# Kernel optimization log

Measured on AMD Instinct MI355X. Metric: run time of the kernel, lower is better.

The kernel has to match this reference:

```python
import jax, jax.numpy as jnp
import numpy as np

MAX_POINTS = 32
EPS = 1e-5


def setup_inputs() -> dict:
    key = jax.random.key(0)
    k1, k2, k3, k4, k5, k6 = jax.random.split(key, 6)
    M, P, C_IN, C_OUT = 40000, MAX_POINTS, 4, 64
    voxel_features = jax.random.normal(k1, (M, P, C_IN), dtype=jnp.float32)
    voxel_num_points = jax.random.randint(k2, (M,), 0, MAX_POINTS, dtype=jnp.int32)
    # Linear(C_in, C_out) params (PyTorch default init scale ~ U(-1/sqrt(fan_in), ...))
    lim = 1.0 / np.sqrt(C_IN)
    W = jax.random.uniform(k3, (C_OUT, C_IN), minval=-lim, maxval=lim, dtype=jnp.float32)
    b = jax.random.uniform(k4, (C_OUT,), minval=-lim, maxval=lim, dtype=jnp.float32)
    # BatchNorm1d affine params
    gamma = jnp.ones((C_OUT,), dtype=jnp.float32)
    beta = jnp.zeros((C_OUT,), dtype=jnp.float32)
    return {"voxel_features": voxel_features, "voxel_num_points": voxel_num_points,
            "W": W, "b": b, "gamma": gamma, "beta": beta}


def _vfe(x, n, W, b, gamma, beta):
    # x: (M, P, C_in), n: (M,) valid point counts
    mask = (jnp.arange(MAX_POINTS)[None, :] < n[:, None])            # (M, P)
    maskf = mask.astype(x.dtype)[..., None]                          # (M, P, 1)
    h = jnp.einsum('mpc,oc->mpo', x, W) + b                          # (M, P, C_out)
    h = h * maskf                                                    # zero invalid slots
    # BatchNorm1d (training-mode batch stats) over valid points only
    n_valid = jnp.maximum(jnp.sum(maskf), 1.0)
    mu = jnp.sum(h, axis=(0, 1)) / n_valid                           # (C_out,)
    d = (h - mu) * maskf
    var = jnp.sum(d * d, axis=(0, 1)) / n_valid                      # biased var, as BN
    hn = d * jax.lax.rsqrt(var + EPS) * gamma + beta * maskf
    hn = jax.nn.relu(hn) * maskf
    # per-voxel mean over valid points; voxels with n==0 output zeros
    counts = jnp.maximum(n.astype(x.dtype), 1.0)[:, None]
    return jnp.sum(hn, axis=1) / counts                              # (M, C_out)


def reference(voxel_features, voxel_num_points, W, b, gamma, beta):
    return _vfe(voxel_features, voxel_num_points, W, b, gamma, beta)
```

## Files before the change

### kernel.cpp

```cpp
#include <hip/hip_runtime.h>

#define MAX_POINTS 32
#define C_OUT 64
#define EPS 1e-5f

#define NMOM 15
#define NSET 8

__global__ __launch_bounds__(256) void vfe_stats(
    const float* __restrict__ x, const int* __restrict__ vnp,
    float* __restrict__ ws, int M)
{
    const int tid    = blockIdx.x * 256 + threadIdx.x;
    const int stride = gridDim.x * 256;
    const int total  = M * MAX_POINTS;

    float a[NMOM];
    #pragma unroll
    for (int i = 0; i < NMOM; ++i) a[i] = 0.f;

    const float4* __restrict__ xq = (const float4*)x;
    for (int i = tid; i < total; i += stride) {
        const float4 q0 = xq[i];
        const int   n   = vnp[i >> 5];
        const float mk  = ((i & 31) < n) ? 1.f : 0.f;
        const float qx = q0.x * mk, qy = q0.y * mk, qz = q0.z * mk, qw = q0.w * mk;
        a[0] += qx; a[1] += qy; a[2] += qz; a[3] += qw;
        a[4]  = fmaf(qx, qx, a[4]);
        a[5]  = fmaf(qx, qy, a[5]);
        a[6]  = fmaf(qx, qz, a[6]);
        a[7]  = fmaf(qx, qw, a[7]);
        a[8]  = fmaf(qy, qy, a[8]);
        a[9]  = fmaf(qy, qz, a[9]);
        a[10] = fmaf(qy, qw, a[10]);
        a[11] = fmaf(qz, qz, a[11]);
        a[12] = fmaf(qz, qw, a[12]);
        a[13] = fmaf(qw, qw, a[13]);
        a[14] += mk;
    }

    #pragma unroll
    for (int i = 0; i < NMOM; ++i) {
        float v = a[i];
        #pragma unroll
        for (int off = 32; off > 0; off >>= 1)
            v += __shfl_down(v, off, 64);
        a[i] = v;
    }

    __shared__ float bl[4][NMOM];
    const int lane = threadIdx.x & 63;
    const int wid  = threadIdx.x >> 6;
    if (lane == 0) {
        #pragma unroll
        for (int i = 0; i < NMOM; ++i) bl[wid][i] = a[i];
    }
    __syncthreads();
    if (threadIdx.x < NMOM) {
        const int i = threadIdx.x;
        const int set = blockIdx.x & (NSET - 1);
        atomicAdd(&ws[set * 16 + i], bl[0][i] + bl[1][i] + bl[2][i] + bl[3][i]);
    }
}

__global__ __launch_bounds__(256) void vfe_out(
    const float* __restrict__ x, const int* __restrict__ vnp,
    const float* __restrict__ W, const float* __restrict__ b,
    const float* __restrict__ gamma, const float* __restrict__ beta,
    const float* __restrict__ ws, float* __restrict__ out, int M)
{
    const int lane = threadIdx.x & 63;
    const int wid  = __builtin_amdgcn_readfirstlane(threadIdx.x >> 6);
    const int gw   = blockIdx.x * 4 + wid;

    float mom[NMOM];
    #pragma unroll
    for (int i = 0; i < NMOM; ++i) {
        float s = 0.f;
        #pragma unroll
        for (int j = 0; j < NSET; ++j) s += ws[j * 16 + i];
        mom[i] = s;
    }

    const float4 w4  = ((const float4*)W)[lane];
    const float bias = b[lane];
    const float cnt  = mom[14];
    const float nv   = fmaxf(cnt, 1.0f);
    const float wdots = w4.x*mom[0] + w4.y*mom[1] + w4.z*mom[2] + w4.w*mom[3];
    const float mu   = (wdots + cnt * bias) / nv;
    const float q2 = mom[4]*w4.x*w4.x + mom[8]*w4.y*w4.y + mom[11]*w4.z*w4.z + mom[13]*w4.w*w4.w
                   + 2.f*(mom[5]*w4.x*w4.y + mom[6]*w4.x*w4.z + mom[7]*w4.x*w4.w
                        + mom[9]*w4.y*w4.z + mom[10]*w4.y*w4.w + mom[12]*w4.z*w4.w);
    const float SS  = q2 + 2.f*bias*wdots + cnt*bias*bias;
    const float var = fmaxf(SS / nv - mu * mu, 0.f);
    const float A   = gamma[lane] * rsqrtf(var + EPS);
    const float B   = fmaf(-mu, A, beta[lane]);

    const int m_base = gw * 8;
    #pragma unroll
    for (int v = 0; v < 8; ++v) {
        const int m = m_base + v;
        if (m >= M) break;
        const int n = vnp[m];
        const float* __restrict__ xr = x + (size_t)m * (MAX_POINTS * 4);
        float acc = 0.f;
        for (int p = 0; p < n; ++p) {
            const float px = xr[p*4+0];
            const float py = xr[p*4+1];
            const float pz = xr[p*4+2];
            const float pw = xr[p*4+3];
            const float h = fmaf(px, w4.x, fmaf(py, w4.y,
                            fmaf(pz, w4.z, fmaf(pw, w4.w, bias))));
            acc += fmaxf(fmaf(h, A, B), 0.f);
        }
        const float rn = 1.0f / fmaxf((float)n, 1.0f);
        out[(size_t)m * C_OUT + lane] = acc * rn;
    }
}

extern "C" void kernel_launch(void* const* d_in, const int* in_sizes, int n_in,
                              void* d_out, int out_size, void* d_ws, size_t ws_size,
                              hipStream_t stream) {
    const float* x     = (const float*)d_in[0];
    const int*   vnp   = (const int*)  d_in[1];
    const float* W     = (const float*)d_in[2];
    const float* b     = (const float*)d_in[3];
    const float* gamma = (const float*)d_in[4];
    const float* beta  = (const float*)d_in[5];
    float* out = (float*)d_out;
    float* ws  = (float*)d_ws;
    const int M = in_sizes[1];

    hipMemsetAsync(d_ws, 0, NSET * 16 * sizeof(float), stream);
    vfe_stats<<<2048, 256, 0, stream>>>(x, vnp, ws, M);
    const int nwaves = (M + 7) / 8;
    const int nblk   = (nwaves + 3) / 4;
    vfe_out<<<nblk, 256, 0, stream>>>(x, vnp, W, b, gamma, beta, ws, out, M);
}
```

Before: 117.9 us.

## Bucket per-voxel point loop into unrolled templates and halve voxels per wave

Replaces the variable-trip per-point loop in the output kernel with templated bodies fully unrolled to 8/16/24/32 points, picked by the voxel's count. The bodies use float4 loads, masking only the last 8 slots, and four independent accumulators. This is meant to remove loop overhead and serialized scalar loads and add memory-level parallelism. Each wave now handles 4 voxels instead of 8, doubling the grid for occupancy. The moment reduction uses float4 reads. Trade-offs are some wasted loads and ALU on masked slots, larger code size, and possible wave divergence when voxels in a wave pick different buckets.

```diff
diff --git a/kernel.cpp b/kernel.cpp
--- a/kernel.cpp
+++ b/kernel.cpp
@@ -63,6 +63,27 @@
     }
 }
 
+template<int NP>
+__device__ __forceinline__ float voxel_body(
+    const float4* __restrict__ xq, int n,
+    float4 w4, float bias, float A, float B)
+{
+    float acc0 = 0.f, acc1 = 0.f, acc2 = 0.f, acc3 = 0.f;
+    #pragma unroll
+    for (int p = 0; p < NP; ++p) {
+        const float4 q = xq[p];
+        const float h = fmaf(q.x, w4.x, fmaf(q.y, w4.y,
+                        fmaf(q.z, w4.z, fmaf(q.w, w4.w, bias))));
+        float v = fmaxf(fmaf(h, A, B), 0.f);
+        if (p >= NP - 8) v = (p < n) ? v : 0.f;
+        if      ((p & 3) == 0) acc0 += v;
+        else if ((p & 3) == 1) acc1 += v;
+        else if ((p & 3) == 2) acc2 += v;
+        else                   acc3 += v;
+    }
+    return (acc0 + acc1) + (acc2 + acc3);
+}
+
 __global__ __launch_bounds__(256) void vfe_out(
     const float* __restrict__ x, const int* __restrict__ vnp,
     const float* __restrict__ W, const float* __restrict__ b,
@@ -70,17 +91,25 @@
     const float* __restrict__ ws, float* __restrict__ out, int M)
 {
     const int lane = threadIdx.x & 63;
-    const int wid  = __builtin_amdgcn_readfirstlane(threadIdx.x >> 6);
+    const int wid  = threadIdx.x >> 6;
     const int gw   = blockIdx.x * 4 + wid;
 
-    float mom[NMOM];
+    const float4* __restrict__ ws4 = (const float4*)ws;
+    float4 m4[4];
     #pragma unroll
-    for (int i = 0; i < NMOM; ++i) {
-        float s = 0.f;
+    for (int k = 0; k < 4; ++k) {
+        float4 s = ws4[k];
         #pragma unroll
-        for (int j = 0; j < NSET; ++j) s += ws[j * 16 + i];
-        mom[i] = s;
+        for (int j = 1; j < NSET; ++j) {
+            const float4 t = ws4[j * 4 + k];
+            s.x += t.x; s.y += t.y; s.z += t.z; s.w += t.w;
+        }
+        m4[k] = s;
     }
+    const float mom[NMOM] = { m4[0].x, m4[0].y, m4[0].z, m4[0].w,
+                              m4[1].x, m4[1].y, m4[1].z, m4[1].w,
+                              m4[2].x, m4[2].y, m4[2].z, m4[2].w,
+                              m4[3].x, m4[3].y, m4[3].z };
 
     const float4 w4  = ((const float4*)W)[lane];
     const float bias = b[lane];
@@ -96,23 +125,19 @@
     const float A   = gamma[lane] * rsqrtf(var + EPS);
     const float B   = fmaf(-mu, A, beta[lane]);
 
-    const int m_base = gw * 8;
+    const int m_base = gw * 4;
     #pragma unroll
-    for (int v = 0; v < 8; ++v) {
+    for (int v = 0; v < 4; ++v) {
         const int m = m_base + v;
         if (m >= M) break;
         const int n = vnp[m];
-        const float* __restrict__ xr = x + (size_t)m * (MAX_POINTS * 4);
-        float acc = 0.f;
-        for (int p = 0; p < n; ++p) {
-            const float px = xr[p*4+0];
-            const float py = xr[p*4+1];
-            const float pz = xr[p*4+2];
-            const float pw = xr[p*4+3];
-            const float h = fmaf(px, w4.x, fmaf(py, w4.y,
-                            fmaf(pz, w4.z, fmaf(pw, w4.w, bias))));
-            acc += fmaxf(fmaf(h, A, B), 0.f);
-        }
+        const float4* __restrict__ xq = (const float4*)x + (size_t)m * MAX_POINTS;
+        float acc;
+        if      (n > 24) acc = voxel_body<32>(xq, n, w4, bias, A, B);
+        else if (n > 16) acc = voxel_body<24>(xq, n, w4, bias, A, B);
+        else if (n >  8) acc = voxel_body<16>(xq, n, w4, bias, A, B);
+        else if (n >  0) acc = voxel_body< 8>(xq, n, w4, bias, A, B);
+        else             acc = 0.f;
         const float rn = 1.0f / fmaxf((float)n, 1.0f);
         out[(size_t)m * C_OUT + lane] = acc * rn;
     }
@@ -133,7 +158,7 @@
 
     hipMemsetAsync(d_ws, 0, NSET * 16 * sizeof(float), stream);
     vfe_stats<<<2048, 256, 0, stream>>>(x, vnp, ws, M);
-    const int nwaves = (M + 7) / 8;
+    const int nwaves = (M + 3) / 4;
     const int nblk   = (nwaves + 3) / 4;
     vfe_out<<<nblk, 256, 0, stream>>>(x, vnp, W, b, gamma, beta, ws, out, M);
 }
```

New measurement: 117.7 us. About the same (-0.2%).
